# Kernel tuning notes

Measured on AMD Instinct MI355X. Metric: run time of the kernel, lower is better.

Reference implementation:

```python
import jax, jax.numpy as jnp
import numpy as np

H, D, RPE_DIM, LAYERS = 8, 64, 64, 3
GAMMA = 0.999  # fixed decay (use_decay=True, requires_grad=False)
EPS = 1e-8

def simple_rmsnorm(x):
    # SimpleRMSNorm: x / (||x||_2 * d^{-1/2} + eps), no learned scale
    rms = jnp.sqrt(jnp.sum(x * x, axis=-1, keepdims=True)) * (x.shape[-1] ** -0.5)
    return x / (rms + EPS)

def rpe_transform(idx, pos_proj_w, pos_proj_b, layer_ws, layer_bs, out_w, out_b):
    # idx: (n, 1) -> (H, n, D)
    x = idx @ pos_proj_w + pos_proj_b            # (n, RPE_DIM)
    for i in range(LAYERS):                       # residual=False -> sequential
        x = jax.nn.relu(simple_rmsnorm(x)) @ layer_ws[i] + layer_bs[i]
    x = jax.nn.relu(simple_rmsnorm(x)) @ out_w + out_b   # (n, H*D)
    n = x.shape[0]
    return x.reshape(n, H, D).transpose(1, 0, 2)  # (H, n, D)

def setup_inputs() -> dict:
    key = jax.random.key(0)
    ks = jax.random.split(key, 6)
    b, n = 8, 4096
    s = RPE_DIM ** -0.5
    return {
        "x": jax.random.normal(ks[0], (b, H, n, D), jnp.float32),
        "pos_proj_w": jax.random.normal(ks[1], (1, RPE_DIM), jnp.float32),
        "pos_proj_b": jnp.zeros((RPE_DIM,), jnp.float32),
        "layer_ws": jax.random.normal(ks[2], (LAYERS, RPE_DIM, RPE_DIM), jnp.float32) * s,
        "layer_bs": jnp.zeros((LAYERS, RPE_DIM), jnp.float32),
        "out_w": jax.random.normal(ks[3], (RPE_DIM, H * D), jnp.float32) * s,
        "out_b": jnp.zeros((H * D,), jnp.float32),
    }

def reference(x, pos_proj_w, pos_proj_b, layer_ws, layer_bs, out_w, out_b):
    b, h, n, d = x.shape
    _rpe = lambda idx: rpe_transform(idx, pos_proj_w, pos_proj_b, layer_ws, layer_bs, out_w, out_b)
    # relative-position kernel values (par_type=1: raw integer offsets)
    zero = _rpe(jnp.zeros((1, 1), x.dtype))                       # (H, 1, D)
    pos_idx = jnp.arange(1, n, dtype=x.dtype).reshape(n - 1, 1)   # 1..n-1
    pos = _rpe(pos_idx)                                           # (H, n-1, D)
    neg = _rpe(-pos_idx[::-1])                                    # -(n-1)..-1
    # fixed exponential decay gamma^|offset|
    coef = jnp.arange(1, n, dtype=x.dtype).reshape(1, n - 1, 1)
    gamma = jnp.full((h, 1, d), GAMMA, x.dtype) ** coef           # (H, n-1, D)
    pos = gamma * pos
    neg = gamma[:, ::-1, :] * neg
    # act_type='none' -> identity activation on a
    a = jnp.concatenate([zero, pos, zero, neg], axis=1)           # (H, 2n, D)
    # circular conv of length 2n realizes the Toeplitz matvec
    y = jnp.fft.rfft(x, n=2 * n, axis=-2)                         # (b,H,n+1?,D) complex
    v = jnp.fft.rfft(a, n=2 * n, axis=-2)[None]                   # (1,H,.,D)
    out = jnp.fft.irfft(v * y, n=2 * n, axis=-2)[:, :, :n, :]
    return out
```

## Files before the change

kernel.cpp:

```cpp
#include <hip/hip_runtime.h>
#include <math.h>

#define NF 8192

__device__ __forceinline__ int phys(int e) { return e ^ (((e >> 4) & 7) << 1); }

__device__ __forceinline__ float2 cmul(float2 a, float2 b) {
    return make_float2(a.x*b.x - a.y*b.y, a.x*b.y + a.y*b.x);
}
__device__ __forceinline__ float2 cmulc(float2 a, float2 b) {
    return make_float2(a.x*b.x + a.y*b.y, a.y*b.x - a.x*b.y);
}
__device__ __forceinline__ float2 cadd(float2 a, float2 b){ return make_float2(a.x+b.x, a.y+b.y); }
__device__ __forceinline__ float2 csub(float2 a, float2 b){ return make_float2(a.x-b.x, a.y-b.y); }
__device__ __forceinline__ float2 mnegi(float2 a){ return make_float2(a.y, -a.x); }
__device__ __forceinline__ float2 mposi(float2 a){ return make_float2(-a.y, a.x); }
#define RSQ2 0.70710678118654752f
__device__ __forceinline__ float2 mw81 (float2 a){ return make_float2( RSQ2*(a.x+a.y),  RSQ2*(a.y-a.x)); }
__device__ __forceinline__ float2 mw83 (float2 a){ return make_float2( RSQ2*(a.y-a.x), -RSQ2*(a.x+a.y)); }
__device__ __forceinline__ float2 mw81c(float2 a){ return make_float2( RSQ2*(a.x-a.y),  RSQ2*(a.x+a.y)); }
__device__ __forceinline__ float2 mw83c(float2 a){ return make_float2(-RSQ2*(a.x+a.y),  RSQ2*(a.x-a.y)); }

#define C16_1 0.92387953251128674f
#define S16_1 0.38268343236508978f
#define C16_2 0.70710678118654752f

__device__ __forceinline__ float2 twbase(int ts) {
    float fa = (float)ts * (1.0f/8192.0f);
    return make_float2(__builtin_amdgcn_cosf(fa), -__builtin_amdgcn_sinf(fa));
}

__device__ __forceinline__ void dif8_core(float2& v0, float2& v1, float2& v2, float2& v3,
                                          float2& v4, float2& v5, float2& v6, float2& v7) {
    float2 t;
    t = csub(v0, v4); v0 = cadd(v0, v4); v4 = t;
    t = csub(v1, v5); v1 = cadd(v1, v5); v5 = mw81(t);
    t = csub(v2, v6); v2 = cadd(v2, v6); v6 = mnegi(t);
    t = csub(v3, v7); v3 = cadd(v3, v7); v7 = mw83(t);
    t = csub(v0, v2); v0 = cadd(v0, v2); v2 = t;
    t = csub(v1, v3); v1 = cadd(v1, v3); v3 = mnegi(t);
    t = csub(v4, v6); v4 = cadd(v4, v6); v6 = t;
    t = csub(v5, v7); v5 = cadd(v5, v7); v7 = mnegi(t);
    t = csub(v0, v1); v0 = cadd(v0, v1); v1 = t;
    t = csub(v2, v3); v2 = cadd(v2, v3); v3 = t;
    t = csub(v4, v5); v4 = cadd(v4, v5); v5 = t;
    t = csub(v6, v7); v6 = cadd(v6, v7); v7 = t;
}

__device__ __forceinline__ void dit8_core(float2& v0, float2& v1, float2& v2, float2& v3,
                                          float2& v4, float2& v5, float2& v6, float2& v7) {
    float2 t;
    t = csub(v0, v1); v0 = cadd(v0, v1); v1 = t;
    t = csub(v2, v3); v2 = cadd(v2, v3); v3 = t;
    t = csub(v4, v5); v4 = cadd(v4, v5); v5 = t;
    t = csub(v6, v7); v6 = cadd(v6, v7); v7 = t;
    t = v2;        v2 = csub(v0, t); v0 = cadd(v0, t);
    t = mposi(v3); v3 = csub(v1, t); v1 = cadd(v1, t);
    t = v6;        v6 = csub(v4, t); v4 = cadd(v4, t);
    t = mposi(v7); v7 = csub(v5, t); v5 = cadd(v5, t);
    t = v4;        v4 = csub(v0, t); v0 = cadd(v0, t);
    t = mw81c(v5); v5 = csub(v1, t); v1 = cadd(v1, t);
    t = mposi(v6); v6 = csub(v2, t); v2 = cadd(v2, t);
    t = mw83c(v7); v7 = csub(v3, t); v3 = cadd(v3, t);
}

#define TW_POWERS(ts) \
    float2 w1 = twbase(ts); \
    float2 w2 = cmul(w1, w1); \
    float2 w3 = cmul(w2, w1); \
    float2 w4 = cmul(w2, w2); \
    float2 w5 = cmul(w3, w2); \
    float2 w6 = cmul(w3, w3); \
    float2 w7 = cmul(w4, w3);

template<int M, int LM>
__device__ __forceinline__ void fwd8_lds(float2* Z, int tid) {
    #pragma unroll
    for (int q = 0; q < 2; ++q) {
        int beta = tid + q*512;
        int i    = beta & (M-1);
        int base = ((beta >> LM) << (LM+3)) + i;
        float2 v0 = Z[phys(base        )];
        float2 v1 = Z[phys(base + 1*M)];
        float2 v2 = Z[phys(base + 2*M)];
        float2 v3 = Z[phys(base + 3*M)];
        float2 v4 = Z[phys(base + 4*M)];
        float2 v5 = Z[phys(base + 5*M)];
        float2 v6 = Z[phys(base + 6*M)];
        float2 v7 = Z[phys(base + 7*M)];
        dif8_core(v0,v1,v2,v3,v4,v5,v6,v7);
        TW_POWERS((NF >> (LM+3)) * i)
        Z[phys(base        )] = v0;
        Z[phys(base + 4*M)] = cmul(v1, w4);
        Z[phys(base + 2*M)] = cmul(v2, w2);
        Z[phys(base + 6*M)] = cmul(v3, w6);
        Z[phys(base + 1*M)] = cmul(v4, w1);
        Z[phys(base + 5*M)] = cmul(v5, w5);
        Z[phys(base + 3*M)] = cmul(v6, w3);
        Z[phys(base + 7*M)] = cmul(v7, w7);
    }
}

template<int M, int LM>
__device__ __forceinline__ void inv8_lds(float2* Z, int tid) {
    #pragma unroll
    for (int q = 0; q < 2; ++q) {
        int beta = tid + q*512;
        int i    = beta & (M-1);
        int base = ((beta >> LM) << (LM+3)) + i;
        TW_POWERS((NF >> (LM+3)) * i)
        float2 v0 = Z[phys(base        )];
        float2 v1 = cmulc(Z[phys(base + 4*M)], w4);
        float2 v2 = cmulc(Z[phys(base + 2*M)], w2);
        float2 v3 = cmulc(Z[phys(base + 6*M)], w6);
        float2 v4 = cmulc(Z[phys(base + 1*M)], w1);
        float2 v5 = cmulc(Z[phys(base + 5*M)], w5);
        float2 v6 = cmulc(Z[phys(base + 3*M)], w3);
        float2 v7 = cmulc(Z[phys(base + 7*M)], w7);
        dit8_core(v0,v1,v2,v3,v4,v5,v6,v7);
        Z[phys(base        )] = v0;
        Z[phys(base + 1*M)] = v1;
        Z[phys(base + 2*M)] = v2;
        Z[phys(base + 3*M)] = v3;
        Z[phys(base + 4*M)] = v4;
        Z[phys(base + 5*M)] = v5;
        Z[phys(base + 6*M)] = v6;
        Z[phys(base + 7*M)] = v7;
    }
}


__global__ __launch_bounds__(512) void rpe_kernel(
    const float* __restrict__ pw,  const float* __restrict__ pb,
    const float* __restrict__ lws, const float* __restrict__ lbs,
    const float* __restrict__ ow,  const float* __restrict__ ob,
    float* __restrict__ a_buf)
{
    __shared__ float sW2[3][32][64][2];
    __shared__ float sWo2[32][64][2];
    __shared__ float sB[3][64];
    __shared__ float sPW[64], sPB[64];
    __shared__ float sAct[8][2][64];
    int tid = threadIdx.x;
    for (int idx = tid; idx < 3*64*64; idx += 512) {
        int L = idx >> 12, rem = idx & 4095, k = rem >> 6, c = rem & 63;
        sW2[L][k >> 1][c][k & 1] = lws[idx];
    }
    if (tid < 192) ((float*)sB)[tid] = lbs[tid];
    if (tid < 64) { sPW[tid] = pw[tid]; sPB[tid] = pb[tid]; }
    __syncthreads();

    int wv = tid >> 6, lane = tid & 63;
    int e0 = blockIdx.x * 16 + wv * 2;
    float xv[2], dec[2];
    #pragma unroll
    for (int s = 0; s < 2; ++s) {
        int e = e0 + s;
        float p = (e == 4096) ? 0.f : ((e < 4096) ? (float)e : (float)(e - 8192));
        int m = (e < 4096) ? e : (8192 - e);
        if (e == 4096) m = 0;
        dec[s] = exp2f(-0.0014434309482562475f * (float)m);
        xv[s] = fmaf(p, sPW[lane], sPB[lane]);
    }

    #pragma unroll
    for (int L = 0; L < 3; ++L) {
        #pragma unroll
        for (int s = 0; s < 2; ++s) {
            float v = xv[s];
            float ss = v * v;
            #pragma unroll
            for (int o = 1; o < 64; o <<= 1) ss += __shfl_xor(ss, o);
            sAct[wv][s][lane] = fmaxf(v / (sqrtf(ss) * 0.125f + 1e-8f), 0.f);
            float y = sB[L][lane];
            const float2* ap = reinterpret_cast<const float2*>(sAct[wv][s]);
            const float2* wp = reinterpret_cast<const float2*>(sW2[L]);
            #pragma unroll
            for (int kk = 0; kk < 32; ++kk) {
                float2 a2 = ap[kk];
                float2 ww = wp[kk*64 + lane];
                y = fmaf(a2.x, ww.x, y);
                y = fmaf(a2.y, ww.y, y);
            }
            xv[s] = y;
        }
    }
    #pragma unroll
    for (int s = 0; s < 2; ++s) {
        float v = xv[s];
        float ss = v * v;
        #pragma unroll
        for (int o = 1; o < 64; o <<= 1) ss += __shfl_xor(ss, o);
        sAct[wv][s][lane] = fmaxf(v / (sqrtf(ss) * 0.125f + 1e-8f), 0.f);
    }
    for (int qq = 0; qq < 8; ++qq) {
        __syncthreads();
        for (int idx = tid; idx < 4096; idx += 512) {
            int k = idx >> 6, c = idx & 63;
            sWo2[k >> 1][c][k & 1] = ow[(size_t)k*512 + qq*64 + c];
        }
        __syncthreads();
        #pragma unroll
        for (int s = 0; s < 2; ++s) {
            float y = ob[qq*64 + lane];
            const float2* ap = reinterpret_cast<const float2*>(sAct[wv][s]);
            const float2* wp = reinterpret_cast<const float2*>(sWo2);
            #pragma unroll
            for (int kk = 0; kk < 32; ++kk) {
                float2 a2 = ap[kk];
                float2 ww = wp[kk*64 + lane];
                y = fmaf(a2.x, ww.x, y);
                y = fmaf(a2.y, ww.y, y);
            }
            a_buf[(size_t)(qq*64 + lane)*NF + (e0 + s)] = y * dec[s];
        }
    }
}

__global__ __launch_bounds__(512, 4) void afft_kernel(
    const float* __restrict__ a_buf, float2* __restrict__ Afft)
{
    __shared__ __align__(16) float2 Z[NF];
    int cc = blockIdx.x, tid = threadIdx.x;
    const float* col = a_buf + (size_t)cc * NF;
    #pragma unroll
    for (int q = 0; q < 2; ++q) {
        int i = tid + q*512;
        float2 v0 = make_float2(col[i       ], 0.f);
        float2 v1 = make_float2(col[i + 1024], 0.f);
        float2 v2 = make_float2(col[i + 2048], 0.f);
        float2 v3 = make_float2(col[i + 3072], 0.f);
        float2 v4 = make_float2(col[i + 4096], 0.f);
        float2 v5 = make_float2(col[i + 5120], 0.f);
        float2 v6 = make_float2(col[i + 6144], 0.f);
        float2 v7 = make_float2(col[i + 7168], 0.f);
        dif8_core(v0,v1,v2,v3,v4,v5,v6,v7);
        TW_POWERS(i)
        Z[phys(i        )] = v0;
        Z[phys(i + 4096)] = cmul(v1, w4);
        Z[phys(i + 2048)] = cmul(v2, w2);
        Z[phys(i + 6144)] = cmul(v3, w6);
        Z[phys(i + 1024)] = cmul(v4, w1);
        Z[phys(i + 5120)] = cmul(v5, w5);
        Z[phys(i + 3072)] = cmul(v6, w3);
        Z[phys(i + 7168)] = cmul(v7, w7);
    }
    __syncthreads();
    fwd8_lds<128, 7>(Z, tid);  __syncthreads();
    fwd8_lds<16,  4>(Z, tid);  __syncthreads();
    {
        int c = tid, sw4 = c & 7;
        float4* Z4 = reinterpret_cast<float4*>(Z);
        float4* oc4 = reinterpret_cast<float4*>(Afft + (size_t)cc * NF);
        float2 z[16];
        #pragma unroll
        for (int j = 0; j < 8; ++j) {
            float4 wv = Z4[c*8 + (j ^ sw4)];
            z[2*j]   = make_float2(wv.x, wv.y);
            z[2*j+1] = make_float2(wv.z, wv.w);
        }
        dif8_core(z[0],z[2],z[4],z[6],z[8],z[10],z[12],z[14]);
        dif8_core(z[1],z[3],z[5],z[7],z[9],z[11],z[13],z[15]);
        #define A4K(k, ZE, ZO, WR, WI) { \
            float2 w = make_float2((WR)*(ZO).x - (WI)*(ZO).y, (WR)*(ZO).y + (WI)*(ZO).x); \
            float2 pp = cadd(ZE, w), rr = csub(ZE, w); \
            oc4[(k)*512 + c] = make_float4(pp.x, pp.y, rr.x, rr.y); }
        { float2 pp = cadd(z[0], z[1]), rr = csub(z[0], z[1]);
          oc4[0*512 + c] = make_float4(pp.x, pp.y, rr.x, rr.y); }
        A4K(1, z[8],  z[9],   C16_1, -S16_1)
        A4K(2, z[4],  z[5],   C16_2, -C16_2)
        A4K(3, z[12], z[13],  S16_1, -C16_1)
        { float2 w = mnegi(z[3]);
          float2 pp = cadd(z[2], w), rr = csub(z[2], w);
          oc4[4*512 + c] = make_float4(pp.x, pp.y, rr.x, rr.y); }
        A4K(5, z[10], z[11], -S16_1, -C16_1)
        A4K(6, z[6],  z[7],  -C16_2, -C16_2)
        A4K(7, z[14], z[15], -C16_1, -S16_1)
        #undef A4K
    }
}

__global__ __launch_bounds__(512, 4) void conv_kernel(
    const float* __restrict__ x, const float2* __restrict__ Afft,
    float* __restrict__ out)
{
    __shared__ __align__(16) float2 Z[NF];
    int blk = blockIdx.x;
    int b   = blk & 7;
    int q   = blk >> 3;
    int h   = q >> 5;
    int dp  = q & 31;
    int tid = threadIdx.x;
    size_t base = ((size_t)(b*8 + h) * 4096) * 64 + 2*dp;

    #pragma unroll
    for (int qq = 0; qq < 2; ++qq) {
        int i = tid + qq*512;
        float2 v0 = *reinterpret_cast<const float2*>(&x[base + (size_t)(i       )*64]);
        float2 v1 = *reinterpret_cast<const float2*>(&x[base + (size_t)(i + 1024)*64]);
        float2 v2 = *reinterpret_cast<const float2*>(&x[base + (size_t)(i + 2048)*64]);
        float2 v3 = *reinterpret_cast<const float2*>(&x[base + (size_t)(i + 3072)*64]);
        float2 v4 = v0;
        float2 v5 = mw81(v1);
        float2 v6 = mnegi(v2);
        float2 v7 = mw83(v3);
        float2 t;
        t = csub(v0, v2); v0 = cadd(v0, v2); v2 = t;
        t = csub(v1, v3); v1 = cadd(v1, v3); v3 = mnegi(t);
        t = csub(v4, v6); v4 = cadd(v4, v6); v6 = t;
        t = csub(v5, v7); v5 = cadd(v5, v7); v7 = mnegi(t);
        t = csub(v0, v1); v0 = cadd(v0, v1); v1 = t;
        t = csub(v2, v3); v2 = cadd(v2, v3); v3 = t;
        t = csub(v4, v5); v4 = cadd(v4, v5); v5 = t;
        t = csub(v6, v7); v6 = cadd(v6, v7); v7 = t;
        TW_POWERS(i)
        Z[phys(i        )] = v0;
        Z[phys(i + 4096)] = cmul(v1, w4);
        Z[phys(i + 2048)] = cmul(v2, w2);
        Z[phys(i + 6144)] = cmul(v3, w6);
        Z[phys(i + 1024)] = cmul(v4, w1);
        Z[phys(i + 5120)] = cmul(v5, w5);
        Z[phys(i + 3072)] = cmul(v6, w3);
        Z[phys(i + 7168)] = cmul(v7, w7);
    }
    __syncthreads();
    fwd8_lds<128, 7>(Z, tid);  __syncthreads();
    fwd8_lds<16,  4>(Z, tid);  __syncthreads();

    {
        int c = tid, sw4 = c & 7;
        int l  = (c >> 6) | (((c >> 3) & 7) << 3) | ((c & 7) << 6);
        int lp = (512 - l) & 511;
        int cp = ((lp & 7) << 6) | (((lp >> 3) & 7) << 3) | (lp >> 6);
        int swp = cp & 7;
        bool l0 = (l == 0);
        float4* Z4 = reinterpret_cast<float4*>(Z);
        const float4* A4a = reinterpret_cast<const float4*>(Afft + (size_t)(h*64 + 2*dp    )*NF);
        const float4* A4b = reinterpret_cast<const float4*>(Afft + (size_t)(h*64 + 2*dp + 1)*NF);

        float2 zz[16];
        #pragma unroll
        for (int j = 0; j < 8; ++j) {
            float4 wv = Z4[c*8 + (j ^ sw4)];
            zz[2*j]   = make_float2(wv.x, wv.y);
            zz[2*j+1] = make_float2(wv.z, wv.w);
        }
        dif8_core(zz[0],zz[2],zz[4],zz[6],zz[8],zz[10],zz[12],zz[14]);
        dif8_core(zz[1],zz[3],zz[5],zz[7],zz[9],zz[11],zz[13],zz[15]);
        float2 S[16];
        #define SPLIT(kk, JE, WR, WI) { \
            float2 E = zz[2*(JE)], O = zz[2*(JE)+1]; \
            float2 wo = make_float2((WR)*O.x - (WI)*O.y, (WR)*O.y + (WI)*O.x); \
            S[kk] = cadd(E, wo); S[(kk)+8] = csub(E, wo); }
        SPLIT(0, 0,  1.0f,   0.0f)
        SPLIT(1, 4,  C16_1, -S16_1)
        SPLIT(2, 2,  C16_2, -C16_2)
        SPLIT(3, 6,  S16_1, -C16_1)
        SPLIT(4, 1,  0.0f,  -1.0f)
        SPLIT(5, 5, -S16_1, -C16_1)
        SPLIT(6, 3, -C16_2, -C16_2)
        SPLIT(7, 7, -C16_1, -S16_1)
        #undef SPLIT
        {
            const int rev3[8] = {0,4,2,6,1,5,3,7};
            #pragma unroll
            for (int j = 0; j < 8; ++j) {
                int m = rev3[j];
                Z4[c*8 + (j ^ sw4)] = make_float4(S[m].x, S[m].y, S[m+8].x, S[m+8].y);
            }
        }
        __syncthreads();
        float2 Sp[16];
        {
            const int rev3[8] = {0,4,2,6,1,5,3,7};
            #pragma unroll
            for (int j = 0; j < 8; ++j) {
                float4 wv = Z4[cp*8 + (j ^ swp)];
                int m = rev3[j];
                Sp[m]   = make_float2(wv.x, wv.y);
                Sp[m+8] = make_float2(wv.z, wv.w);
            }
        }
        float2 Yv[16];
        #define YPAIR(kk, IA0, IB0, IA8, IB8) { \
            float4 aa = A4a[(kk)*512 + c]; \
            float4 ab = A4b[(kk)*512 + c]; \
            { float2 P = l0 ? Sp[IA0] : Sp[IB0]; \
              float2 E = make_float2(0.5f*(S[kk].x + P.x),  0.5f*(S[kk].y - P.y)); \
              float2 O = make_float2(0.5f*(S[kk].y + P.y), -0.5f*(S[kk].x - P.x)); \
              Yv[kk] = cadd(cmul(E, make_float2(aa.x, aa.y)), mposi(cmul(O, make_float2(ab.x, ab.y)))); } \
            { float2 P = l0 ? Sp[IA8] : Sp[IB8]; \
              float2 E = make_float2(0.5f*(S[(kk)+8].x + P.x),  0.5f*(S[(kk)+8].y - P.y)); \
              float2 O = make_float2(0.5f*(S[(kk)+8].y + P.y), -0.5f*(S[(kk)+8].x - P.x)); \
              Yv[(kk)+8] = cadd(cmul(E, make_float2(aa.z, aa.w)), mposi(cmul(O, make_float2(ab.z, ab.w)))); } }
        YPAIR(0,  0, 15, 8, 7)
        YPAIR(1, 15, 14, 7, 6)
        YPAIR(2, 14, 13, 6, 5)
        YPAIR(3, 13, 12, 5, 4)
        YPAIR(4, 12, 11, 4, 3)
        YPAIR(5, 11, 10, 3, 2)
        YPAIR(6, 10,  9, 2, 1)
        YPAIR(7,  9,  8, 1, 0)
        #undef YPAIR
        #define GPAIR(kk, JE, WRC, WIC) { \
            float2 GE = cadd(Yv[kk], Yv[(kk)+8]); \
            float2 GO = csub(Yv[kk], Yv[(kk)+8]); \
            zz[2*(JE)]   = GE; \
            zz[2*(JE)+1] = make_float2((WRC)*GO.x - (WIC)*GO.y, (WRC)*GO.y + (WIC)*GO.x); }
        GPAIR(0, 0,  1.0f,  0.0f)
        GPAIR(1, 4,  C16_1, S16_1)
        GPAIR(2, 2,  C16_2, C16_2)
        GPAIR(3, 6,  S16_1, C16_1)
        GPAIR(4, 1,  0.0f,  1.0f)
        GPAIR(5, 5, -S16_1, C16_1)
        GPAIR(6, 3, -C16_2, C16_2)
        GPAIR(7, 7, -C16_1, S16_1)
        #undef GPAIR
        dit8_core(zz[0],zz[2],zz[4],zz[6],zz[8],zz[10],zz[12],zz[14]);
        dit8_core(zz[1],zz[3],zz[5],zz[7],zz[9],zz[11],zz[13],zz[15]);
        __syncthreads();
        #pragma unroll
        for (int j = 0; j < 8; ++j)
            Z4[c*8 + (j ^ sw4)] = make_float4(zz[2*j].x, zz[2*j].y, zz[2*j+1].x, zz[2*j+1].y);
    }
    __syncthreads();
    inv8_lds<16,  4>(Z, tid);  __syncthreads();
    inv8_lds<128, 7>(Z, tid);  __syncthreads();

    const float sc = 1.0f/8192.0f;
    #pragma unroll
    for (int qq = 0; qq < 2; ++qq) {
        int i = tid + qq*512;
        TW_POWERS(i)
        float2 v0 = Z[phys(i        )];
        float2 v1 = cmulc(Z[phys(i + 4096)], w4);
        float2 v2 = cmulc(Z[phys(i + 2048)], w2);
        float2 v3 = cmulc(Z[phys(i + 6144)], w6);
        float2 v4 = cmulc(Z[phys(i + 1024)], w1);
        float2 v5 = cmulc(Z[phys(i + 5120)], w5);
        float2 v6 = cmulc(Z[phys(i + 3072)], w3);
        float2 v7 = cmulc(Z[phys(i + 7168)], w7);
        float2 t;
        t = csub(v0, v1); v0 = cadd(v0, v1); v1 = t;
        t = csub(v2, v3); v2 = cadd(v2, v3); v3 = t;
        t = csub(v4, v5); v4 = cadd(v4, v5); v5 = t;
        t = csub(v6, v7); v6 = cadd(v6, v7); v7 = t;
        t = v2;        v2 = csub(v0, t); v0 = cadd(v0, t);
        t = mposi(v3); v3 = csub(v1, t); v1 = cadd(v1, t);
        t = v6;        v6 = csub(v4, t); v4 = cadd(v4, t);
        t = mposi(v7); v7 = csub(v5, t); v5 = cadd(v5, t);
        v0 = cadd(v0, v4);
        v1 = cadd(v1, mw81c(v5));
        v2 = cadd(v2, mposi(v6));
        v3 = cadd(v3, mw83c(v7));
        *reinterpret_cast<float2*>(&out[base + (size_t)(i       )*64]) = make_float2(v0.x*sc, v0.y*sc);
        *reinterpret_cast<float2*>(&out[base + (size_t)(i + 1024)*64]) = make_float2(v1.x*sc, v1.y*sc);
        *reinterpret_cast<float2*>(&out[base + (size_t)(i + 2048)*64]) = make_float2(v2.x*sc, v2.y*sc);
        *reinterpret_cast<float2*>(&out[base + (size_t)(i + 3072)*64]) = make_float2(v3.x*sc, v3.y*sc);
    }
}

extern "C" void kernel_launch(void* const* d_in, const int* in_sizes, int n_in,
                              void* d_out, int out_size, void* d_ws, size_t ws_size,
                              hipStream_t stream) {
    const float* x   = (const float*)d_in[0];
    const float* pw  = (const float*)d_in[1];
    const float* pb  = (const float*)d_in[2];
    const float* lws = (const float*)d_in[3];
    const float* lbs = (const float*)d_in[4];
    const float* ow  = (const float*)d_in[5];
    const float* ob  = (const float*)d_in[6];
    float* out = (float*)d_out;
    char* ws = (char*)d_ws;
    float*  a_buf = (float*)ws;
    float2* Afft  = (float2*)(ws + (size_t)512*NF*4);

    rpe_kernel<<<512, 512, 0, stream>>>(pw, pb, lws, lbs, ow, ob, a_buf);
    afft_kernel<<<512, 512, 0, stream>>>(a_buf, Afft);
    conv_kernel<<<2048, 512, 0, stream>>>(x, Afft, out);
}
```

Baseline: 495.5 us.

## Process four channels per conv block with float4 global loads and stores

The conv kernel now handles four adjacent D channels per block instead of two. It loads and stores x/out as float4 and runs the FFT-convolve-IFFT body twice through a shared helper function. This halves the number of blocks and widens global accesses to improve coalescing on the strided x/out layout. In exchange each thread holds more registers (input and output arrays for both pairs), which could reduce occupancy, and the two FFT passes run serially within a block.

Result: slower. 617.9 us (+24.7%).

```diff
diff --git a/kernel.cpp b/kernel.cpp
--- a/kernel.cpp
+++ b/kernel.cpp
@@ -129,177 +129,18 @@
     }
 }
 
-
-__global__ __launch_bounds__(512) void rpe_kernel(
-    const float* __restrict__ pw,  const float* __restrict__ pb,
-    const float* __restrict__ lws, const float* __restrict__ lbs,
-    const float* __restrict__ ow,  const float* __restrict__ ob,
-    float* __restrict__ a_buf)
+__device__ __forceinline__ void fft_conv_split(
+    float2* __restrict__ Z, int tid,
+    const float4* __restrict__ A4a, const float4* __restrict__ A4b,
+    const float2 (&vin)[8], float2 (&vout)[8])
 {
-    __shared__ float sW2[3][32][64][2];
-    __shared__ float sWo2[32][64][2];
-    __shared__ float sB[3][64];
-    __shared__ float sPW[64], sPB[64];
-    __shared__ float sAct[8][2][64];
-    int tid = threadIdx.x;
-    for (int idx = tid; idx < 3*64*64; idx += 512) {
-        int L = idx >> 12, rem = idx & 4095, k = rem >> 6, c = rem & 63;
-        sW2[L][k >> 1][c][k & 1] = lws[idx];
-    }
-    if (tid < 192) ((float*)sB)[tid] = lbs[tid];
-    if (tid < 64) { sPW[tid] = pw[tid]; sPB[tid] = pb[tid]; }
-    __syncthreads();
-
-    int wv = tid >> 6, lane = tid & 63;
-    int e0 = blockIdx.x * 16 + wv * 2;
-    float xv[2], dec[2];
-    #pragma unroll
-    for (int s = 0; s < 2; ++s) {
-        int e = e0 + s;
-        float p = (e == 4096) ? 0.f : ((e < 4096) ? (float)e : (float)(e - 8192));
-        int m = (e < 4096) ? e : (8192 - e);
-        if (e == 4096) m = 0;
-        dec[s] = exp2f(-0.0014434309482562475f * (float)m);
-        xv[s] = fmaf(p, sPW[lane], sPB[lane]);
-    }
-
-    #pragma unroll
-    for (int L = 0; L < 3; ++L) {
-        #pragma unroll
-        for (int s = 0; s < 2; ++s) {
-            float v = xv[s];
-            float ss = v * v;
-            #pragma unroll
-            for (int o = 1; o < 64; o <<= 1) ss += __shfl_xor(ss, o);
-            sAct[wv][s][lane] = fmaxf(v / (sqrtf(ss) * 0.125f + 1e-8f), 0.f);
-            float y = sB[L][lane];
-            const float2* ap = reinterpret_cast<const float2*>(sAct[wv][s]);
-            const float2* wp = reinterpret_cast<const float2*>(sW2[L]);
-            #pragma unroll
-            for (int kk = 0; kk < 32; ++kk) {
-                float2 a2 = ap[kk];
-                float2 ww = wp[kk*64 + lane];
-                y = fmaf(a2.x, ww.x, y);
-                y = fmaf(a2.y, ww.y, y);
-            }
-            xv[s] = y;
-        }
-    }
-    #pragma unroll
-    for (int s = 0; s < 2; ++s) {
-        float v = xv[s];
-        float ss = v * v;
-        #pragma unroll
-        for (int o = 1; o < 64; o <<= 1) ss += __shfl_xor(ss, o);
-        sAct[wv][s][lane] = fmaxf(v / (sqrtf(ss) * 0.125f + 1e-8f), 0.f);
-    }
-    for (int qq = 0; qq < 8; ++qq) {
-        __syncthreads();
-        for (int idx = tid; idx < 4096; idx += 512) {
-            int k = idx >> 6, c = idx & 63;
-            sWo2[k >> 1][c][k & 1] = ow[(size_t)k*512 + qq*64 + c];
-        }
-        __syncthreads();
-        #pragma unroll
-        for (int s = 0; s < 2; ++s) {
-            float y = ob[qq*64 + lane];
-            const float2* ap = reinterpret_cast<const float2*>(sAct[wv][s]);
-            const float2* wp = reinterpret_cast<const float2*>(sWo2);
-            #pragma unroll
-            for (int kk = 0; kk < 32; ++kk) {
-                float2 a2 = ap[kk];
-                float2 ww = wp[kk*64 + lane];
-                y = fmaf(a2.x, ww.x, y);
-                y = fmaf(a2.y, ww.y, y);
-            }
-            a_buf[(size_t)(qq*64 + lane)*NF + (e0 + s)] = y * dec[s];
-        }
-    }
-}
-
-__global__ __launch_bounds__(512, 4) void afft_kernel(
-    const float* __restrict__ a_buf, float2* __restrict__ Afft)
-{
-    __shared__ __align__(16) float2 Z[NF];
-    int cc = blockIdx.x, tid = threadIdx.x;
-    const float* col = a_buf + (size_t)cc * NF;
-    #pragma unroll
-    for (int q = 0; q < 2; ++q) {
-        int i = tid + q*512;
-        float2 v0 = make_float2(col[i       ], 0.f);
-        float2 v1 = make_float2(col[i + 1024], 0.f);
-        float2 v2 = make_float2(col[i + 2048], 0.f);
-        float2 v3 = make_float2(col[i + 3072], 0.f);
-        float2 v4 = make_float2(col[i + 4096], 0.f);
-        float2 v5 = make_float2(col[i + 5120], 0.f);
-        float2 v6 = make_float2(col[i + 6144], 0.f);
-        float2 v7 = make_float2(col[i + 7168], 0.f);
-        dif8_core(v0,v1,v2,v3,v4,v5,v6,v7);
-        TW_POWERS(i)
-        Z[phys(i        )] = v0;
-        Z[phys(i + 4096)] = cmul(v1, w4);
-        Z[phys(i + 2048)] = cmul(v2, w2);
-        Z[phys(i + 6144)] = cmul(v3, w6);
-        Z[phys(i + 1024)] = cmul(v4, w1);
-        Z[phys(i + 5120)] = cmul(v5, w5);
-        Z[phys(i + 3072)] = cmul(v6, w3);
-        Z[phys(i + 7168)] = cmul(v7, w7);
-    }
-    __syncthreads();
-    fwd8_lds<128, 7>(Z, tid);  __syncthreads();
-    fwd8_lds<16,  4>(Z, tid);  __syncthreads();
-    {
-        int c = tid, sw4 = c & 7;
-        float4* Z4 = reinterpret_cast<float4*>(Z);
-        float4* oc4 = reinterpret_cast<float4*>(Afft + (size_t)cc * NF);
-        float2 z[16];
-        #pragma unroll
-        for (int j = 0; j < 8; ++j) {
-            float4 wv = Z4[c*8 + (j ^ sw4)];
-            z[2*j]   = make_float2(wv.x, wv.y);
-            z[2*j+1] = make_float2(wv.z, wv.w);
-        }
-        dif8_core(z[0],z[2],z[4],z[6],z[8],z[10],z[12],z[14]);
-        dif8_core(z[1],z[3],z[5],z[7],z[9],z[11],z[13],z[15]);
-        #define A4K(k, ZE, ZO, WR, WI) { \
-            float2 w = make_float2((WR)*(ZO).x - (WI)*(ZO).y, (WR)*(ZO).y + (WI)*(ZO).x); \
-            float2 pp = cadd(ZE, w), rr = csub(ZE, w); \
-            oc4[(k)*512 + c] = make_float4(pp.x, pp.y, rr.x, rr.y); }
-        { float2 pp = cadd(z[0], z[1]), rr = csub(z[0], z[1]);
-          oc4[0*512 + c] = make_float4(pp.x, pp.y, rr.x, rr.y); }
-        A4K(1, z[8],  z[9],   C16_1, -S16_1)
-        A4K(2, z[4],  z[5],   C16_2, -C16_2)
-        A4K(3, z[12], z[13],  S16_1, -C16_1)
-        { float2 w = mnegi(z[3]);
-          float2 pp = cadd(z[2], w), rr = csub(z[2], w);
-          oc4[4*512 + c] = make_float4(pp.x, pp.y, rr.x, rr.y); }
-        A4K(5, z[10], z[11], -S16_1, -C16_1)
-        A4K(6, z[6],  z[7],  -C16_2, -C16_2)
-        A4K(7, z[14], z[15], -C16_1, -S16_1)
-        #undef A4K
-    }
-}
-
-__global__ __launch_bounds__(512, 4) void conv_kernel(
-    const float* __restrict__ x, const float2* __restrict__ Afft,
-    float* __restrict__ out)
-{
-    __shared__ __align__(16) float2 Z[NF];
-    int blk = blockIdx.x;
-    int b   = blk & 7;
-    int q   = blk >> 3;
-    int h   = q >> 5;
-    int dp  = q & 31;
-    int tid = threadIdx.x;
-    size_t base = ((size_t)(b*8 + h) * 4096) * 64 + 2*dp;
-
     #pragma unroll
     for (int qq = 0; qq < 2; ++qq) {
         int i = tid + qq*512;
-        float2 v0 = *reinterpret_cast<const float2*>(&x[base + (size_t)(i       )*64]);
-        float2 v1 = *reinterpret_cast<const float2*>(&x[base + (size_t)(i + 1024)*64]);
-        float2 v2 = *reinterpret_cast<const float2*>(&x[base + (size_t)(i + 2048)*64]);
-        float2 v3 = *reinterpret_cast<const float2*>(&x[base + (size_t)(i + 3072)*64]);
+        float2 v0 = vin[qq*4+0];
+        float2 v1 = vin[qq*4+1];
+        float2 v2 = vin[qq*4+2];
+        float2 v3 = vin[qq*4+3];
         float2 v4 = v0;
         float2 v5 = mw81(v1);
         float2 v6 = mnegi(v2);
@@ -335,8 +176,6 @@
         int swp = cp & 7;
         bool l0 = (l == 0);
         float4* Z4 = reinterpret_cast<float4*>(Z);
-        const float4* A4a = reinterpret_cast<const float4*>(Afft + (size_t)(h*64 + 2*dp    )*NF);
-        const float4* A4b = reinterpret_cast<const float4*>(Afft + (size_t)(h*64 + 2*dp + 1)*NF);
 
         float2 zz[16];
         #pragma unroll
@@ -427,7 +266,6 @@
     inv8_lds<16,  4>(Z, tid);  __syncthreads();
     inv8_lds<128, 7>(Z, tid);  __syncthreads();
 
-    const float sc = 1.0f/8192.0f;
     #pragma unroll
     for (int qq = 0; qq < 2; ++qq) {
         int i = tid + qq*512;
@@ -449,14 +287,210 @@
         t = mposi(v3); v3 = csub(v1, t); v1 = cadd(v1, t);
         t = v6;        v6 = csub(v4, t); v4 = cadd(v4, t);
         t = mposi(v7); v7 = csub(v5, t); v5 = cadd(v5, t);
-        v0 = cadd(v0, v4);
-        v1 = cadd(v1, mw81c(v5));
-        v2 = cadd(v2, mposi(v6));
-        v3 = cadd(v3, mw83c(v7));
-        *reinterpret_cast<float2*>(&out[base + (size_t)(i       )*64]) = make_float2(v0.x*sc, v0.y*sc);
-        *reinterpret_cast<float2*>(&out[base + (size_t)(i + 1024)*64]) = make_float2(v1.x*sc, v1.y*sc);
-        *reinterpret_cast<float2*>(&out[base + (size_t)(i + 2048)*64]) = make_float2(v2.x*sc, v2.y*sc);
-        *reinterpret_cast<float2*>(&out[base + (size_t)(i + 3072)*64]) = make_float2(v3.x*sc, v3.y*sc);
+        vout[qq*4+0] = cadd(v0, v4);
+        vout[qq*4+1] = cadd(v1, mw81c(v5));
+        vout[qq*4+2] = cadd(v2, mposi(v6));
+        vout[qq*4+3] = cadd(v3, mw83c(v7));
+    }
+}
+
+
+__global__ __launch_bounds__(512) void rpe_kernel(
+    const float* __restrict__ pw,  const float* __restrict__ pb,
+    const float* __restrict__ lws, const float* __restrict__ lbs,
+    const float* __restrict__ ow,  const float* __restrict__ ob,
+    float* __restrict__ a_buf)
+{
+    __shared__ float sW2[3][32][64][2];
+    __shared__ float sWo2[32][64][2];
+    __shared__ float sB[3][64];
+    __shared__ float sPW[64], sPB[64];
+    __shared__ float sAct[8][2][64];
+    int tid = threadIdx.x;
+    for (int idx = tid; idx < 3*64*64; idx += 512) {
+        int L = idx >> 12, rem = idx & 4095, k = rem >> 6, c = rem & 63;
+        sW2[L][k >> 1][c][k & 1] = lws[idx];
+    }
+    if (tid < 192) ((float*)sB)[tid] = lbs[tid];
+    if (tid < 64) { sPW[tid] = pw[tid]; sPB[tid] = pb[tid]; }
+    __syncthreads();
+
+    int wv = tid >> 6, lane = tid & 63;
+    int e0 = blockIdx.x * 16 + wv * 2;
+    float xv[2], dec[2];
+    #pragma unroll
+    for (int s = 0; s < 2; ++s) {
+        int e = e0 + s;
+        float p = (e == 4096) ? 0.f : ((e < 4096) ? (float)e : (float)(e - 8192));
+        int m = (e < 4096) ? e : (8192 - e);
+        if (e == 4096) m = 0;
+        dec[s] = exp2f(-0.0014434309482562475f * (float)m);
+        xv[s] = fmaf(p, sPW[lane], sPB[lane]);
+    }
+
+    #pragma unroll
+    for (int L = 0; L < 3; ++L) {
+        #pragma unroll
+        for (int s = 0; s < 2; ++s) {
+            float v = xv[s];
+            float ss = v * v;
+            #pragma unroll
+            for (int o = 1; o < 64; o <<= 1) ss += __shfl_xor(ss, o);
+            sAct[wv][s][lane] = fmaxf(v / (sqrtf(ss) * 0.125f + 1e-8f), 0.f);
+            float y = sB[L][lane];
+            const float2* ap = reinterpret_cast<const float2*>(sAct[wv][s]);
+            const float2* wp = reinterpret_cast<const float2*>(sW2[L]);
+            #pragma unroll
+            for (int kk = 0; kk < 32; ++kk) {
+                float2 a2 = ap[kk];
+                float2 ww = wp[kk*64 + lane];
+                y = fmaf(a2.x, ww.x, y);
+                y = fmaf(a2.y, ww.y, y);
+            }
+            xv[s] = y;
+        }
+    }
+    #pragma unroll
+    for (int s = 0; s < 2; ++s) {
+        float v = xv[s];
+        float ss = v * v;
+        #pragma unroll
+        for (int o = 1; o < 64; o <<= 1) ss += __shfl_xor(ss, o);
+        sAct[wv][s][lane] = fmaxf(v / (sqrtf(ss) * 0.125f + 1e-8f), 0.f);
+    }
+    for (int qq = 0; qq < 8; ++qq) {
+        __syncthreads();
+        for (int idx = tid; idx < 4096; idx += 512) {
+            int k = idx >> 6, c = idx & 63;
+            sWo2[k >> 1][c][k & 1] = ow[(size_t)k*512 + qq*64 + c];
+        }
+        __syncthreads();
+        #pragma unroll
+        for (int s = 0; s < 2; ++s) {
+            float y = ob[qq*64 + lane];
+            const float2* ap = reinterpret_cast<const float2*>(sAct[wv][s]);
+            const float2* wp = reinterpret_cast<const float2*>(sWo2);
+            #pragma unroll
+            for (int kk = 0; kk < 32; ++kk) {
+                float2 a2 = ap[kk];
+                float2 ww = wp[kk*64 + lane];
+                y = fmaf(a2.x, ww.x, y);
+                y = fmaf(a2.y, ww.y, y);
+            }
+            a_buf[(size_t)(qq*64 + lane)*NF + (e0 + s)] = y * dec[s];
+        }
+    }
+}
+
+__global__ __launch_bounds__(512, 4) void afft_kernel(
+    const float* __restrict__ a_buf, float2* __restrict__ Afft)
+{
+    __shared__ __align__(16) float2 Z[NF];
+    int cc = blockIdx.x, tid = threadIdx.x;
+    const float* col = a_buf + (size_t)cc * NF;
+    #pragma unroll
+    for (int q = 0; q < 2; ++q) {
+        int i = tid + q*512;
+        float2 v0 = make_float2(col[i       ], 0.f);
+        float2 v1 = make_float2(col[i + 1024], 0.f);
+        float2 v2 = make_float2(col[i + 2048], 0.f);
+        float2 v3 = make_float2(col[i + 3072], 0.f);
+        float2 v4 = make_float2(col[i + 4096], 0.f);
+        float2 v5 = make_float2(col[i + 5120], 0.f);
+        float2 v6 = make_float2(col[i + 6144], 0.f);
+        float2 v7 = make_float2(col[i + 7168], 0.f);
+        dif8_core(v0,v1,v2,v3,v4,v5,v6,v7);
+        TW_POWERS(i)
+        Z[phys(i        )] = v0;
+        Z[phys(i + 4096)] = cmul(v1, w4);
+        Z[phys(i + 2048)] = cmul(v2, w2);
+        Z[phys(i + 6144)] = cmul(v3, w6);
+        Z[phys(i + 1024)] = cmul(v4, w1);
+        Z[phys(i + 5120)] = cmul(v5, w5);
+        Z[phys(i + 3072)] = cmul(v6, w3);
+        Z[phys(i + 7168)] = cmul(v7, w7);
+    }
+    __syncthreads();
+    fwd8_lds<128, 7>(Z, tid);  __syncthreads();
+    fwd8_lds<16,  4>(Z, tid);  __syncthreads();
+    {
+        int c = tid, sw4 = c & 7;
+        float4* Z4 = reinterpret_cast<float4*>(Z);
+        float4* oc4 = reinterpret_cast<float4*>(Afft + (size_t)cc * NF);
+        float2 z[16];
+        #pragma unroll
+        for (int j = 0; j < 8; ++j) {
+            float4 wv = Z4[c*8 + (j ^ sw4)];
+            z[2*j]   = make_float2(wv.x, wv.y);
+            z[2*j+1] = make_float2(wv.z, wv.w);
+        }
+        dif8_core(z[0],z[2],z[4],z[6],z[8],z[10],z[12],z[14]);
+        dif8_core(z[1],z[3],z[5],z[7],z[9],z[11],z[13],z[15]);
+        #define A4K(k, ZE, ZO, WR, WI) { \
+            float2 w = make_float2((WR)*(ZO).x - (WI)*(ZO).y, (WR)*(ZO).y + (WI)*(ZO).x); \
+            float2 pp = cadd(ZE, w), rr = csub(ZE, w); \
+            oc4[(k)*512 + c] = make_float4(pp.x, pp.y, rr.x, rr.y); }
+        { float2 pp = cadd(z[0], z[1]), rr = csub(z[0], z[1]);
+          oc4[0*512 + c] = make_float4(pp.x, pp.y, rr.x, rr.y); }
+        A4K(1, z[8],  z[9],   C16_1, -S16_1)
+        A4K(2, z[4],  z[5],   C16_2, -C16_2)
+        A4K(3, z[12], z[13],  S16_1, -C16_1)
+        { float2 w = mnegi(z[3]);
+          float2 pp = cadd(z[2], w), rr = csub(z[2], w);
+          oc4[4*512 + c] = make_float4(pp.x, pp.y, rr.x, rr.y); }
+        A4K(5, z[10], z[11], -S16_1, -C16_1)
+        A4K(6, z[6],  z[7],  -C16_2, -C16_2)
+        A4K(7, z[14], z[15], -C16_1, -S16_1)
+        #undef A4K
+    }
+}
+
+__global__ __launch_bounds__(512, 4) void conv_kernel(
+    const float* __restrict__ x, const float2* __restrict__ Afft,
+    float* __restrict__ out)
+{
+    __shared__ __align__(16) float2 Z[NF];
+    int blk = blockIdx.x;
+    int b   = blk & 7;
+    int qb  = blk >> 3;
+    int h   = qb >> 4;
+    int dq  = qb & 15;
+    int d0  = dq * 4;
+    int tid = threadIdx.x;
+    size_t base = ((size_t)(b*8 + h) * 4096) * 64 + d0;
+
+    float2 inA[8], inB[8];
+    #pragma unroll
+    for (int qq = 0; qq < 2; ++qq) {
+        #pragma unroll
+        for (int l = 0; l < 4; ++l) {
+            int p = tid + qq*512 + l*1024;
+            float4 f = *reinterpret_cast<const float4*>(&x[base + (size_t)p*64]);
+            inA[qq*4+l] = make_float2(f.x, f.y);
+            inB[qq*4+l] = make_float2(f.z, f.w);
+        }
+    }
+
+    const float4* A4a = reinterpret_cast<const float4*>(Afft + (size_t)(h*64 + d0    )*NF);
+    const float4* A4b = reinterpret_cast<const float4*>(Afft + (size_t)(h*64 + d0 + 1)*NF);
+    const float4* A4c = reinterpret_cast<const float4*>(Afft + (size_t)(h*64 + d0 + 2)*NF);
+    const float4* A4d = reinterpret_cast<const float4*>(Afft + (size_t)(h*64 + d0 + 3)*NF);
+
+    float2 outA[8], outB[8];
+    fft_conv_split(Z, tid, A4a, A4b, inA, outA);
+    __syncthreads();
+    fft_conv_split(Z, tid, A4c, A4d, inB, outB);
+
+    const float sc = 1.0f/8192.0f;
+    #pragma unroll
+    for (int qq = 0; qq < 2; ++qq) {
+        #pragma unroll
+        for (int l = 0; l < 4; ++l) {
+            int p = tid + qq*512 + l*1024;
+            float2 yA = outA[qq*4+l], yB = outB[qq*4+l];
+            *reinterpret_cast<float4*>(&out[base + (size_t)p*64]) =
+                make_float4(yA.x*sc, yA.y*sc, yB.x*sc, yB.y*sc);
+        }
     }
 }
 
@@ -477,5 +511,5 @@
 
     rpe_kernel<<<512, 512, 0, stream>>>(pw, pb, lws, lbs, ow, ob, a_buf);
     afft_kernel<<<512, 512, 0, stream>>>(a_buf, Afft);
-    conv_kernel<<<2048, 512, 0, stream>>>(x, Afft, out);
-}
+    conv_kernel<<<1024, 512, 0, stream>>>(x, Afft, out);
+}
```
